# Kernel optimization log

Measured on AMD Instinct MI355X. Metric: run time of the kernel, lower is better.

## Reference

```python
import jax, jax.numpy as jnp
import numpy as np

B = 2; D = 256; NH = 8; NL = 4; HD = D // NH
K = 2; P = K * K; NV = 4; DFF = 1024
SHAPES = ((128, 128), (64, 64), (32, 32), (16, 16))
LV = sum(h * w for h, w in SHAPES)
START = np.cumsum([0] + [h * w for h, w in SHAPES])[:-1].tolist()
EPS = 1e-5

# fixed 2x2 sampling kernel, matching _create_kernel_indices (even kernel branch)
_ind = np.linspace(-0.5, 0.5, K)
_ii, _jj = np.meshgrid(_ind, _ind, indexing='ij')
KERNEL = jnp.asarray(np.stack([_jj, _ii], -1).reshape(-1, 2) / K, jnp.float32)  # (P,2)


def _layer_norm(x, w, b):
    m = x.mean(-1, keepdims=True)
    v = ((x - m) ** 2).mean(-1, keepdims=True)
    return (x - m) * jax.lax.rsqrt(v + EPS) * w + b


def _box_attention(query, value, ref_windows, vpw, vpb, opw, opb, boxw, boxb, attw, attb):
    b, lq, _ = query.shape
    # value projection, split into heads: (b, NH, LV, HD)
    v = (value @ vpw.T + vpb).reshape(b, LV, NH, HD).transpose(0, 2, 1, 3)

    # attention weights: softmax over all (level, point) jointly per head
    aw = query @ attw.T + attb
    aw = jax.nn.softmax(aw.reshape(b, lq, NH, NL * P), -1).reshape(b, lq, NH, NL, P)

    # where to attend (with_rotation=False -> 4 offset variables, angle from ref)
    ob = (query @ boxw.T + boxb).reshape(b, lq, NH, NL, NV)
    rw = ref_windows[:, :, None, None, :]                    # (b,lq,1,1,7)
    ref_boxes = rw[..., jnp.array([0, 1, 3, 4])]
    angles = jnp.broadcast_to(rw[..., 6:7], (b, lq, NH, NL, 1))
    boxes = ref_boxes + ob / 8.0 * ref_boxes[..., jnp.array([2, 3, 2, 3])]
    center = boxes[..., None, :2]                            # (b,lq,NH,NL,1,2)
    size = boxes[..., None, 2:]
    c, s = jnp.cos(angles), jnp.sin(angles)
    rot = jnp.stack([c, -s, s, c], -1).reshape(b, lq, NH, NL, 1, 2, 2)
    g = KERNEL * jax.nn.relu(size)                           # (b,lq,NH,NL,P,2)
    grid = center + (g[..., None, :] * rot).sum(-1)          # (b,lq,NH,NL,P,2)

    # multi-level bilinear sampling (= grid_sample align_corners=False, zero pad)
    bidx = jnp.arange(b)[:, None, None, None]
    hidx = jnp.arange(NH)[None, None, :, None]
    out = jnp.zeros((b, lq, NH, HD), v.dtype)
    for lvl, (H, W) in enumerate(SHAPES):
        st = START[lvl]
        vl = v[:, :, st:st + H * W]                          # (b,NH,HW,HD)
        loc = grid[:, :, :, lvl]                             # (b,lq,NH,P,2)
        x = loc[..., 0] * W - 0.5
        y = loc[..., 1] * H - 0.5
        x0f = jnp.floor(x); y0f = jnp.floor(y)
        wx = x - x0f; wy = y - y0f
        x0 = x0f.astype(jnp.int32); y0 = y0f.astype(jnp.int32)
        acc = jnp.zeros((b, lq, NH, P, HD), v.dtype)
        corners = ((0, 0, (1 - wx) * (1 - wy)), (1, 0, wx * (1 - wy)),
                   (0, 1, (1 - wx) * wy), (1, 1, wx * wy))
        for dx, dy, wgt in corners:
            xi = x0 + dx; yi = y0 + dy
            valid = (xi >= 0) & (xi < W) & (yi >= 0) & (yi < H)
            idx = jnp.clip(yi, 0, H - 1) * W + jnp.clip(xi, 0, W - 1)
            samp = vl[bidx, hidx, idx]                       # (b,lq,NH,P,HD)
            acc = acc + (wgt * valid)[..., None] * samp
        out = out + jnp.einsum('blhp,blhpd->blhd', aw[:, :, :, lvl], acc)
    return out.reshape(b, lq, D) @ opw.T + opb


def setup_inputs() -> dict:
    key = jax.random.key(0)
    ks = jax.random.split(key, 20)
    def nrm(k, shape, fan_in):
        return jax.random.normal(k, shape, jnp.float32) * (1.0 / np.sqrt(fan_in))
    rw = jax.random.uniform(ks[2], (B, LV, 7), jnp.float32)
    # keep window sizes (cols 3,4,5) modest, like real BEV reference windows
    rw = rw.at[..., 3:6].multiply(0.2)
    return {
        'src': jax.random.normal(ks[0], (B, LV, D), jnp.float32),
        'pos': jax.random.normal(ks[1], (B, LV, D), jnp.float32),
        'src_shape': jnp.asarray(SHAPES, jnp.int32),
        'src_start_idx': jnp.asarray(START, jnp.int32),
        'ref_windows': rw,
        'vpw': nrm(ks[3], (D, D), D), 'vpb': jnp.zeros((D,), jnp.float32),
        'opw': nrm(ks[4], (D, D), D), 'opb': jnp.zeros((D,), jnp.float32),
        'boxw': nrm(ks[5], (NL * NH * NV, D), D) * 0.1,
        'boxb': jax.random.normal(ks[6], (NL * NH * NV,), jnp.float32) * 0.1,
        'attw': nrm(ks[7], (NH * NL * P, D), D),
        'attb': jnp.zeros((NH * NL * P,), jnp.float32),
        'lin1_w': nrm(ks[8], (DFF, D), D), 'lin1_b': jnp.zeros((DFF,), jnp.float32),
        'lin2_w': nrm(ks[9], (D, DFF), DFF), 'lin2_b': jnp.zeros((D,), jnp.float32),
        'ln1_w': jnp.ones((D,), jnp.float32), 'ln1_b': jnp.zeros((D,), jnp.float32),
        'ln2_w': jnp.ones((D,), jnp.float32), 'ln2_b': jnp.zeros((D,), jnp.float32),
    }


def reference(src, pos, src_shape, src_start_idx, ref_windows,
              vpw, vpb, opw, opb, boxw, boxb, attw, attb,
              lin1_w, lin1_b, lin2_w, lin2_b, ln1_w, ln1_b, ln2_w, ln2_b):
    # level shapes/starts are static (SHAPES/START constants); src_shape /
    # src_start_idx are accepted for signature fidelity.
    src2 = _box_attention(src + pos, src, ref_windows,
                          vpw, vpb, opw, opb, boxw, boxb, attw, attb)
    src = _layer_norm(src + src2, ln1_w, ln1_b)
    ffn = jax.nn.relu(src @ lin1_w.T + lin1_b) @ lin2_w.T + lin2_b
    return _layer_norm(src + ffn, ln2_w, ln2_b)
```

## Files before the change

kernel.cpp:

```cpp
#include <hip/hip_runtime.h>
#include <stdint.h>

typedef unsigned short u16;
typedef __attribute__((ext_vector_type(8))) short short8;
typedef __attribute__((ext_vector_type(4))) float f32x4;

#define D_    256
#define NH_   8
#define HD_   32
#define LV_   21760
#define DFF_  1024
#define EPS_  1e-5f
#define MH_   21760
#define MT_   43520

__device__ __forceinline__ float bf2f(u16 u) {
    union { uint32_t i; float f; } x; x.i = ((uint32_t)u) << 16; return x.f;
}
__device__ __forceinline__ u16 f2bf(float f) {
    union { float f; uint32_t i; } x; x.f = f;
    uint32_t r = x.i + 0x7FFFu + ((x.i >> 16) & 1u);
    return (u16)(r >> 16);
}
__device__ __forceinline__ uint32_t pk2(float a, float b) {
    return (uint32_t)f2bf(a) | ((uint32_t)f2bf(b) << 16);
}
__device__ __forceinline__ float blo(uint32_t u) {
    union { uint32_t i; float f; } x; x.i = u << 16; return x.f;
}
__device__ __forceinline__ float bhi(uint32_t u) {
    union { uint32_t i; float f; } x; x.i = u & 0xffff0000u; return x.f;
}
__device__ __forceinline__ void cv8(u16* dst, float4 a, float4 b) {
    uint4 r;
    r.x = pk2(a.x, a.y); r.y = pk2(a.z, a.w);
    r.z = pk2(b.x, b.y); r.w = pk2(b.z, b.w);
    *(uint4*)dst = r;
}
__device__ __forceinline__ void gload16(const u16* g, u16* l) {
    __builtin_amdgcn_global_load_lds(
        (const __attribute__((address_space(1))) uint32_t*)g,
        (__attribute__((address_space(3))) uint32_t*)l, 16, 0, 0);
}

__global__ __launch_bounds__(256) void k_cvt2(const float* __restrict__ in1, u16* __restrict__ out1,
                                              const float* __restrict__ in2, u16* __restrict__ out2) {
    int i = blockIdx.x * 256 + threadIdx.x;
    const float* in = (i < 65536) ? in1 : in2;
    u16* out = (i < 65536) ? out1 : out2;
    const int j = i & 65535;
    float4 v = ((const float4*)in)[j];
    uint2 r; r.x = pk2(v.x, v.y); r.y = pk2(v.z, v.w);
    *(uint2*)(out + (size_t)j * 4) = r;
}

__global__ __launch_bounds__(256) void k_proj(
        const float* __restrict__ src, const float* __restrict__ pos,
        const float* __restrict__ vpw, const float* __restrict__ vpb,
        const float* __restrict__ attw, const float* __restrict__ attb,
        const float* __restrict__ boxw, const float* __restrict__ boxb,
        u16* __restrict__ vout, u16* __restrict__ lgout) {
    __shared__ u16 As[2][64 * 32];
    __shared__ u16 Bs[2][64 * 32];
    const int t = threadIdx.x;
    const int l = t & 63, w = t >> 6;
    const int m0 = blockIdx.x * 64;
    const int by = blockIdx.y;
    const bool isv = by < 4;
    const int n0 = (by & 3) * 64;
    const float* Bsrc = isv ? (vpw + (size_t)n0 * 256)
                            : ((n0 < 128) ? (attw + (size_t)n0 * 256)
                                          : (boxw + (size_t)(n0 - 128) * 256));
    const float* bsrc = isv ? (vpb + n0)
                            : ((n0 < 128) ? (attb + n0) : (boxb + (n0 - 128)));
    const int sr = t >> 2, sc = t & 3;
    const int wslot = sr * 32 + ((sc ^ ((sr >> 1) & 3)) << 3);
    const float* gAs = src + (size_t)(m0 + sr) * 256 + sc * 8;
    const float* gAp = pos + (size_t)(m0 + sr) * 256 + sc * 8;
    const float* gB  = Bsrc + (size_t)sr * 256 + sc * 8;
    const int fr = l & 15, fg = l >> 4;
    const int wm = w >> 1, wn = w & 1;

    f32x4 acc[2][2];
    #pragma unroll
    for (int mi = 0; mi < 2; ++mi)
        #pragma unroll
        for (int ni = 0; ni < 2; ++ni)
            acc[mi][ni] = (f32x4){0.f, 0.f, 0.f, 0.f};

    {
        float4 a0 = *(const float4*)gAs, a1 = *(const float4*)(gAs + 4);
        if (!isv) {
            float4 p0 = *(const float4*)gAp, p1 = *(const float4*)(gAp + 4);
            a0.x += p0.x; a0.y += p0.y; a0.z += p0.z; a0.w += p0.w;
            a1.x += p1.x; a1.y += p1.y; a1.z += p1.z; a1.w += p1.w;
        }
        cv8(&As[0][wslot], a0, a1);
        cv8(&Bs[0][wslot], *(const float4*)gB, *(const float4*)(gB + 4));
    }
    __syncthreads();

    for (int kt = 0; kt < 8; ++kt) {
        const int cur = kt & 1;
        float4 na0, na1, nb0, nb1;
        if (kt < 7) {
            na0 = *(const float4*)(gAs + (kt + 1) * 32);
            na1 = *(const float4*)(gAs + (kt + 1) * 32 + 4);
            if (!isv) {
                float4 p0 = *(const float4*)(gAp + (kt + 1) * 32);
                float4 p1 = *(const float4*)(gAp + (kt + 1) * 32 + 4);
                na0.x += p0.x; na0.y += p0.y; na0.z += p0.z; na0.w += p0.w;
                na1.x += p1.x; na1.y += p1.y; na1.z += p1.z; na1.w += p1.w;
            }
            nb0 = *(const float4*)(gB + (kt + 1) * 32);
            nb1 = *(const float4*)(gB + (kt + 1) * 32 + 4);
        }
        short8 af[2], bfr[2];
        #pragma unroll
        for (int mi = 0; mi < 2; ++mi) {
            const int r = wm * 32 + mi * 16 + fr;
            af[mi] = *(const short8*)&As[cur][r * 32 + ((fg ^ ((r >> 1) & 3)) << 3)];
        }
        #pragma unroll
        for (int ni = 0; ni < 2; ++ni) {
            const int r = wn * 32 + ni * 16 + fr;
            bfr[ni] = *(const short8*)&Bs[cur][r * 32 + ((fg ^ ((r >> 1) & 3)) << 3)];
        }
        #pragma unroll
        for (int mi = 0; mi < 2; ++mi)
            #pragma unroll
            for (int ni = 0; ni < 2; ++ni)
                acc[mi][ni] = __builtin_amdgcn_mfma_f32_16x16x32_bf16(af[mi], bfr[ni], acc[mi][ni], 0, 0, 0);
        if (kt < 7) {
            cv8(&As[cur ^ 1][wslot], na0, na1);
            cv8(&Bs[cur ^ 1][wslot], nb0, nb1);
            __syncthreads();
        }
    }
    if (isv) {
        const int b = m0 / LV_;
        #pragma unroll
        for (int ni = 0; ni < 2; ++ni) {
            const int n = n0 + wn * 32 + ni * 16 + fr;
            const float bv = bsrc[wn * 32 + ni * 16 + fr];
            const int h = n >> 5, hd = n & 31;
            #pragma unroll
            for (int mi = 0; mi < 2; ++mi) {
                #pragma unroll
                for (int q = 0; q < 4; ++q) {
                    const int m = m0 + wm * 32 + mi * 16 + fg * 4 + q;
                    const int lrow = m - b * LV_;
                    vout[((size_t)(b * NH_ + h) * LV_ + lrow) * HD_ + hd] = f2bf(acc[mi][ni][q] + bv);
                }
            }
        }
    } else {
        #pragma unroll
        for (int ni = 0; ni < 2; ++ni) {
            const int nl_ = wn * 32 + ni * 16 + fr;
            const int n = n0 + nl_;
            const float bv = bsrc[nl_];
            const int off = (n < 128) ? ((n >> 4) * 32 + (n & 15))
                                      : (((n - 128) >> 4) * 32 + 16 + ((n - 128) & 15));
            #pragma unroll
            for (int mi = 0; mi < 2; ++mi) {
                #pragma unroll
                for (int q = 0; q < 4; ++q) {
                    const int m = m0 + wm * 32 + mi * 16 + fg * 4 + q;
                    lgout[(size_t)m * 256 + off] = f2bf(acc[mi][ni][q] + bv);
                }
            }
        }
    }
}

__global__ __launch_bounds__(128, 8) void k_sample(
        const u16* __restrict__ lg, const float* __restrict__ refw,
        const u16* __restrict__ vws, u16* __restrict__ smp) {
    __shared__ float LG[8][2][36];
    __shared__ float RW[8][8];
    __shared__ __align__(16) uint2 CWI[16 * 68];
    const int t = threadIdx.x;
    const int bid = blockIdx.x;
    const int combo = bid & 7;
    const int idx = bid >> 3;
    const int b = combo >> 2, hp = combo & 3;
    const int h0 = hp * 2;
    const long gr0 = (long)b * LV_ + (long)idx * 8;
    const uint32_t PLANEB = (uint32_t)LV_ * HD_ * 2;

    {
        const int row = t >> 4, part = t & 15;
        const uint2 v = *(const uint2*)(lg + (size_t)(gr0 + row) * 256 + h0 * 32 + part * 4);
        const int hs = part >> 3, kk = (part & 7) * 4;
        LG[row][hs][kk]     = blo(v.x);
        LG[row][hs][kk + 1] = bhi(v.x);
        LG[row][hs][kk + 2] = blo(v.y);
        LG[row][hs][kk + 3] = bhi(v.y);
        if (t < 56) {
            int r2 = t / 7, k = t % 7;
            RW[r2][k] = refw[(gr0 + r2) * 7 + k];
        }
    }
    __syncthreads();
    if (t < 16) {
        const int row = t >> 1, hs = t & 1;
        float* a = LG[row][hs];
        float m = a[0];
        #pragma unroll
        for (int k = 1; k < 16; ++k) m = fmaxf(m, a[k]);
        float s = 0.f;
        float e[16];
        #pragma unroll
        for (int k = 0; k < 16; ++k) { e[k] = __expf(a[k] - m); s += e[k]; }
        const float inv = 1.f / s;
        #pragma unroll
        for (int k = 0; k < 16; ++k) a[k] = e[k] * inv;
    }
    __syncthreads();
    #pragma unroll
    for (int uu = 0; uu < 2; ++uu) {
        const int u = t + uu * 128;
        const int row = u >> 5, rem = u & 31;
        const int hs = rem >> 4, nl = (rem >> 2) & 3, p = rem & 3;
        const float rw0 = RW[row][0], rw1 = RW[row][1], rw3 = RW[row][3], rw4 = RW[row][4], ang = RW[row][6];
        const float ob0 = LG[row][hs][16 + nl * 4 + 0];
        const float ob1 = LG[row][hs][16 + nl * 4 + 1];
        const float ob2 = LG[row][hs][16 + nl * 4 + 2];
        const float ob3 = LG[row][hs][16 + nl * 4 + 3];
        const float cx = rw0 + ob0 * 0.125f * rw3;
        const float cy = rw1 + ob1 * 0.125f * rw4;
        const float bw = fmaxf(rw3 + ob2 * 0.125f * rw3, 0.f);
        const float bh = fmaxf(rw4 + ob3 * 0.125f * rw4, 0.f);
        const float kx = (p & 1) ? 0.25f : -0.25f;
        const float ky = (p >> 1) ? 0.25f : -0.25f;
        float sth, cth;
        __sincosf(ang, &sth, &cth);
        const float g0 = kx * bw, g1 = ky * bh;
        const float gx = cx + g0 * cth - g1 * sth;
        const float gy = cy + g0 * sth + g1 * cth;
        const int Wl = 128 >> nl;
        const int st = (65536 - (65536 >> (2 * nl))) / 3;
        const float x = gx * Wl - 0.5f, y = gy * Wl - 0.5f;
        const float xf = floorf(x), yf = floorf(y);
        const float wx = x - xf, wy = y - yf;
        const int x0 = (int)xf, y0 = (int)yf;
        const float awv = LG[row][hs][nl * 4 + p];
        const uint32_t hoff = hs ? PLANEB : 0u;
        uint2 cw[4];
        #pragma unroll
        for (int c4 = 0; c4 < 4; ++c4) {
            const int dx = c4 & 1, dy = c4 >> 1;
            const int xi = x0 + dx, yi = y0 + dy;
            const float wgt = (dx ? wx : 1.f - wx) * (dy ? wy : 1.f - wy);
            const bool valid = (xi >= 0) && (xi < Wl) && (yi >= 0) && (yi < Wl);
            const int xc = xi < 0 ? 0 : (xi > Wl - 1 ? Wl - 1 : xi);
            const int yc = yi < 0 ? 0 : (yi > Wl - 1 ? Wl - 1 : yi);
            const float wv = valid ? wgt * awv : 0.f;
            cw[c4].x = __float_as_uint(wv);
            cw[c4].y = (uint32_t)(st + yc * Wl + xc) * 64u + hoff;
        }
        const int g = row * 2 + hs, un = nl * 4 + p;
        uint2* d0 = &CWI[g * 68 + un * 2];
        *(uint4*)(d0)      = *(const uint4*)&cw[0];
        *(uint4*)(d0 + 34) = *(const uint4*)&cw[2];
    }
    __syncthreads();
    {
        const int e = t & 7, g = t >> 3;
        const int row = g >> 1, hs = g & 1;
        const char* vbp = (const char*)vws +
            (((size_t)(b * NH_ + h0) * LV_) * HD_ + e * 4) * 2;
        const uint2* cbase = &CWI[g * 68];
        float a0 = 0.f, a1 = 0.f, a2 = 0.f, a3 = 0.f;
        #pragma unroll 1
        for (int k = 0; k < 16; k += 2) {
            const uint4 c0 = *(const uint4*)&cbase[k * 2];
            const uint4 c1 = *(const uint4*)&cbase[34 + k * 2];
            const uint4 c2 = *(const uint4*)&cbase[(k + 1) * 2];
            const uint4 c3 = *(const uint4*)&cbase[34 + (k + 1) * 2];
            const uint2 d0 = *(const uint2*)(vbp + c0.y);
            const uint2 d1 = *(const uint2*)(vbp + c0.w);
            const uint2 d2 = *(const uint2*)(vbp + c1.y);
            const uint2 d3 = *(const uint2*)(vbp + c1.w);
            const uint2 d4 = *(const uint2*)(vbp + c2.y);
            const uint2 d5 = *(const uint2*)(vbp + c2.w);
            const uint2 d6 = *(const uint2*)(vbp + c3.y);
            const uint2 d7 = *(const uint2*)(vbp + c3.w);
            #define ACC8(WB, DD) do { \
                const float w_ = __uint_as_float(WB); \
                a0 += w_ * blo((DD).x); a1 += w_ * bhi((DD).x); \
                a2 += w_ * blo((DD).y); a3 += w_ * bhi((DD).y); \
            } while (0)
            ACC8(c0.x, d0); ACC8(c0.z, d1); ACC8(c1.x, d2); ACC8(c1.z, d3);
            ACC8(c2.x, d4); ACC8(c2.z, d5); ACC8(c3.x, d6); ACC8(c3.z, d7);
            #undef ACC8
        }
        uint2 o; o.x = pk2(a0, a1); o.y = pk2(a2, a3);
        *(uint2*)(smp + (size_t)(gr0 + row) * 256 + (h0 + hs) * 32 + e * 4) = o;
    }
}

__global__ __launch_bounds__(256) void k_oproj(
        const u16* __restrict__ A,
        const float* __restrict__ opw,
        const float* __restrict__ opb,
        const float* __restrict__ src,
        const float* __restrict__ lnw, const float* __restrict__ lnb,
        u16* __restrict__ out) {
    __shared__ char smem[36864];
    u16* As = (u16*)smem;
    u16* Bs = (u16*)(smem + 4096);
    float* Y = (float*)smem;
    const int t = threadIdx.x;
    const int l = t & 63, w = t >> 6;
    const int m0 = blockIdx.x * 32;
    const int sAr = t >> 2, sc = t & 3;
    const int aslot = sAr * 32 + ((sc ^ ((sAr >> 1) & 3)) << 3);
    const u16* gA = A + (size_t)(m0 + sAr) * 256 + sc * 8;
    const float* gB[4];
    int bslot[4];
    #pragma unroll
    for (int i = 0; i < 4; ++i) {
        const int r = (t >> 2) + i * 64;
        gB[i] = opw + (size_t)r * 256 + sc * 8;
        bslot[i] = r * 32 + ((sc ^ ((r >> 1) & 3)) << 3);
    }
    const int fr = l & 15, fg = l >> 4;

    f32x4 acc[2][4];
    #pragma unroll
    for (int mi = 0; mi < 2; ++mi)
        #pragma unroll
        for (int ni = 0; ni < 4; ++ni)
            acc[mi][ni] = (f32x4){0.f, 0.f, 0.f, 0.f};

    if (t < 128) *(uint4*)&As[aslot] = *(const uint4*)gA;
    #pragma unroll
    for (int i = 0; i < 4; ++i)
        cv8(&Bs[bslot[i]], *(const float4*)gB[i], *(const float4*)(gB[i] + 4));
    __syncthreads();

    for (int kt = 0; kt < 8; ++kt) {
        const int cur = kt & 1;
        uint4 na; float4 nb[4][2];
        if (kt < 7) {
            if (t < 128) na = *(const uint4*)(gA + (kt + 1) * 32);
            #pragma unroll
            for (int i = 0; i < 4; ++i) {
                nb[i][0] = *(const float4*)(gB[i] + (kt + 1) * 32);
                nb[i][1] = *(const float4*)(gB[i] + (kt + 1) * 32 + 4);
            }
        }
        short8 af[2], bfr[4];
        #pragma unroll
        for (int mi = 0; mi < 2; ++mi) {
            const int r = mi * 16 + fr;
            af[mi] = *(const short8*)&As[cur * 1024 + r * 32 + ((fg ^ ((r >> 1) & 3)) << 3)];
        }
        #pragma unroll
        for (int ni = 0; ni < 4; ++ni) {
            const int r = w * 64 + ni * 16 + fr;
            bfr[ni] = *(const short8*)&Bs[cur * 8192 + r * 32 + ((fg ^ ((r >> 1) & 3)) << 3)];
        }
        #pragma unroll
        for (int mi = 0; mi < 2; ++mi)
            #pragma unroll
            for (int ni = 0; ni < 4; ++ni)
                acc[mi][ni] = __builtin_amdgcn_mfma_f32_16x16x32_bf16(af[mi], bfr[ni], acc[mi][ni], 0, 0, 0);
        if (kt < 7) {
            if (t < 128) *(uint4*)&As[(cur ^ 1) * 1024 + aslot] = na;
            #pragma unroll
            for (int i = 0; i < 4; ++i)
                cv8(&Bs[(cur ^ 1) * 8192 + bslot[i]], nb[i][0], nb[i][1]);
            __syncthreads();
        }
    }
    __syncthreads();
    #pragma unroll
    for (int ni = 0; ni < 4; ++ni) {
        const int n = w * 64 + ni * 16 + fr;
        const float bv = opb[n];
        #pragma unroll
        for (int mi = 0; mi < 2; ++mi) {
            #pragma unroll
            for (int q = 0; q < 4; ++q) {
                const int ml = mi * 16 + fg * 4 + q;
                Y[ml * 256 + n] = acc[mi][ni][q] + bv + src[(size_t)(m0 + ml) * 256 + n];
            }
        }
    }
    __syncthreads();
    for (int rr = 0; rr < 8; ++rr) {
        const int m = w * 8 + rr;
        const float v0 = Y[m * 256 + l];
        const float v1 = Y[m * 256 + 64 + l];
        const float v2 = Y[m * 256 + 128 + l];
        const float v3 = Y[m * 256 + 192 + l];
        float s1 = v0 + v1 + v2 + v3;
        float s2 = v0 * v0 + v1 * v1 + v2 * v2 + v3 * v3;
        #pragma unroll
        for (int off = 32; off; off >>= 1) {
            s1 += __shfl_xor(s1, off);
            s2 += __shfl_xor(s2, off);
        }
        const float mean = s1 * (1.f / 256.f);
        const float var = s2 * (1.f / 256.f) - mean * mean;
        const float rs = rsqrtf(var + EPS_);
        const size_t ob = (size_t)(m0 + m) * 256;
        out[ob + l]       = f2bf((v0 - mean) * rs * lnw[l]       + lnb[l]);
        out[ob + 64 + l]  = f2bf((v1 - mean) * rs * lnw[64 + l]  + lnb[64 + l]);
        out[ob + 128 + l] = f2bf((v2 - mean) * rs * lnw[128 + l] + lnb[128 + l]);
        out[ob + 192 + l] = f2bf((v3 - mean) * rs * lnw[192 + l] + lnb[192 + l]);
    }
}

__global__ __launch_bounds__(256) void k_gemm1(
        const u16* __restrict__ A, const u16* __restrict__ Bw,
        const float* __restrict__ bias, u16* __restrict__ H) {
    __shared__ u16 As[2][128 * 32];
    __shared__ u16 Bs[2][128 * 32];
    const int t = threadIdx.x;
    const int l = t & 63, w = t >> 6;
    const int m0 = blockIdx.x * 128, n0 = blockIdx.y * 128;
    const int r0 = t >> 2, c0 = t & 3;
    const int gc = c0 ^ ((r0 >> 1) & 3);
    const u16* gA0 = A  + (size_t)(m0 + r0) * 256 + gc * 8;
    const u16* gA1 = A  + (size_t)(m0 + r0 + 64) * 256 + gc * 8;
    const u16* gB0 = Bw + (size_t)(n0 + r0) * 256 + gc * 8;
    const u16* gB1 = Bw + (size_t)(n0 + r0 + 64) * 256 + gc * 8;
    const int lbase = w * 512;
    const int fr = l & 15, fg = l >> 4;
    const int wm = w >> 1, wn = w & 1;

    f32x4 acc[4][4];
    #pragma unroll
    for (int mi = 0; mi < 4; ++mi)
        #pragma unroll
        for (int ni = 0; ni < 4; ++ni)
            acc[mi][ni] = (f32x4){0.f, 0.f, 0.f, 0.f};

    #define STAGE1(buf, kt) do { \
        gload16(gA0 + (kt) * 32, &As[buf][lbase]); \
        gload16(gA1 + (kt) * 32, &As[buf][2048 + lbase]); \
        gload16(gB0 + (kt) * 32, &Bs[buf][lbase]); \
        gload16(gB1 + (kt) * 32, &Bs[buf][2048 + lbase]); \
    } while (0)

    STAGE1(0, 0);
    __syncthreads();

    for (int kt = 0; kt < 8; ++kt) {
        const int cur = kt & 1;
        if (kt < 7) STAGE1(cur ^ 1, kt + 1);
        short8 af[4], bfr[4];
        #pragma unroll
        for (int mi = 0; mi < 4; ++mi) {
            const int r = wm * 64 + mi * 16 + fr;
            af[mi] = *(const short8*)&As[cur][r * 32 + ((fg ^ ((r >> 1) & 3)) << 3)];
        }
        #pragma unroll
        for (int ni = 0; ni < 4; ++ni) {
            const int r = wn * 64 + ni * 16 + fr;
            bfr[ni] = *(const short8*)&Bs[cur][r * 32 + ((fg ^ ((r >> 1) & 3)) << 3)];
        }
        #pragma unroll
        for (int mi = 0; mi < 4; ++mi)
            #pragma unroll
            for (int ni = 0; ni < 4; ++ni)
                acc[mi][ni] = __builtin_amdgcn_mfma_f32_16x16x32_bf16(af[mi], bfr[ni], acc[mi][ni], 0, 0, 0);
        __syncthreads();
    }
    #undef STAGE1
    #pragma unroll
    for (int ni = 0; ni < 4; ++ni) {
        const int n = n0 + wn * 64 + ni * 16 + fr;
        const float bv = bias[n];
        #pragma unroll
        for (int mi = 0; mi < 4; ++mi) {
            #pragma unroll
            for (int q = 0; q < 4; ++q) {
                const int m = m0 + wm * 64 + mi * 16 + fg * 4 + q;
                const float v = acc[mi][ni][q] + bv;
                H[(size_t)m * 1024 + n] = f2bf(fmaxf(v, 0.f));
            }
        }
    }
}

__global__ __launch_bounds__(256) void k_gemm2(
        const u16* __restrict__ A, const u16* __restrict__ Bw,
        const float* __restrict__ bias, const u16* __restrict__ resid,
        const float* __restrict__ lnw, const float* __restrict__ lnb,
        float* __restrict__ out) {
    __shared__ char smem[36864];
    u16* As = (u16*)smem;
    u16* Bs = (u16*)(smem + 4096);
    float* Y = (float*)smem;
    const int t = threadIdx.x;
    const int l = t & 63, w = t >> 6;
    const int m0 = blockIdx.x * 32;
    const int r0 = t >> 2, c0 = t & 3;
    const int gc = c0 ^ ((r0 >> 1) & 3);
    const u16* gA = A + (size_t)(m0 + r0) * 1024 + gc * 8;
    const u16* gBp[4];
    #pragma unroll
    for (int i = 0; i < 4; ++i)
        gBp[i] = Bw + (size_t)(i * 64 + r0) * 1024 + gc * 8;
    const int lbase = w * 512;
    const int fr = l & 15, fg = l >> 4;

    f32x4 acc[2][4];
    #pragma unroll
    for (int mi = 0; mi < 2; ++mi)
        #pragma unroll
        for (int ni = 0; ni < 4; ++ni)
            acc[mi][ni] = (f32x4){0.f, 0.f, 0.f, 0.f};

    #define STAGE2(buf, kt) do { \
        if (t < 128) gload16(gA + (kt) * 32, &As[(buf) * 1024 + lbase]); \
        gload16(gBp[0] + (kt) * 32, &Bs[(buf) * 8192 + lbase]); \
        gload16(gBp[1] + (kt) * 32, &Bs[(buf) * 8192 + 2048 + lbase]); \
        gload16(gBp[2] + (kt) * 32, &Bs[(buf) * 8192 + 4096 + lbase]); \
        gload16(gBp[3] + (kt) * 32, &Bs[(buf) * 8192 + 6144 + lbase]); \
    } while (0)

    STAGE2(0, 0);
    __syncthreads();

    for (int kt = 0; kt < 32; ++kt) {
        const int cur = kt & 1;
        if (kt < 31) STAGE2(cur ^ 1, kt + 1);
        short8 af[2], bfr[4];
        #pragma unroll
        for (int mi = 0; mi < 2; ++mi) {
            const int r = mi * 16 + fr;
            af[mi] = *(const short8*)&As[cur * 1024 + r * 32 + ((fg ^ ((r >> 1) & 3)) << 3)];
        }
        #pragma unroll
        for (int ni = 0; ni < 4; ++ni) {
            const int r = w * 64 + ni * 16 + fr;
            bfr[ni] = *(const short8*)&Bs[cur * 8192 + r * 32 + ((fg ^ ((r >> 1) & 3)) << 3)];
        }
        #pragma unroll
        for (int mi = 0; mi < 2; ++mi)
            #pragma unroll
            for (int ni = 0; ni < 4; ++ni)
                acc[mi][ni] = __builtin_amdgcn_mfma_f32_16x16x32_bf16(af[mi], bfr[ni], acc[mi][ni], 0, 0, 0);
        __syncthreads();
    }
    #undef STAGE2
    #pragma unroll
    for (int ni = 0; ni < 4; ++ni) {
        const int n = w * 64 + ni * 16 + fr;
        const float bv = bias[n];
        #pragma unroll
        for (int mi = 0; mi < 2; ++mi) {
            #pragma unroll
            for (int q = 0; q < 4; ++q) {
                const int ml = mi * 16 + fg * 4 + q;
                Y[ml * 256 + n] = acc[mi][ni][q] + bv + bf2f(resid[(size_t)(m0 + ml) * 256 + n]);
            }
        }
    }
    __syncthreads();
    for (int rr = 0; rr < 8; ++rr) {
        const int m = w * 8 + rr;
        const float v0 = Y[m * 256 + l];
        const float v1 = Y[m * 256 + 64 + l];
        const float v2 = Y[m * 256 + 128 + l];
        const float v3 = Y[m * 256 + 192 + l];
        float s1 = v0 + v1 + v2 + v3;
        float s2 = v0 * v0 + v1 * v1 + v2 * v2 + v3 * v3;
        #pragma unroll
        for (int off = 32; off; off >>= 1) {
            s1 += __shfl_xor(s1, off);
            s2 += __shfl_xor(s2, off);
        }
        const float mean = s1 * (1.f / 256.f);
        const float var = s2 * (1.f / 256.f) - mean * mean;
        const float rs = rsqrtf(var + EPS_);
        const size_t ob = (size_t)(m0 + m) * 256;
        out[ob + l]        = (v0 - mean) * rs * lnw[l]        + lnb[l];
        out[ob + 64 + l]   = (v1 - mean) * rs * lnw[64 + l]   + lnb[64 + l];
        out[ob + 128 + l]  = (v2 - mean) * rs * lnw[128 + l]  + lnb[128 + l];
        out[ob + 192 + l]  = (v3 - mean) * rs * lnw[192 + l]  + lnb[192 + l];
    }
}

extern "C" void kernel_launch(void* const* d_in, const int* in_sizes, int n_in,
                              void* d_out, int out_size, void* d_ws, size_t ws_size,
                              hipStream_t stream) {
    const float* src  = (const float*)d_in[0];
    const float* pos  = (const float*)d_in[1];
    const float* refw = (const float*)d_in[4];
    const float* vpw  = (const float*)d_in[5];
    const float* vpb  = (const float*)d_in[6];
    const float* opw  = (const float*)d_in[7];
    const float* opb  = (const float*)d_in[8];
    const float* boxw = (const float*)d_in[9];
    const float* boxb = (const float*)d_in[10];
    const float* attw = (const float*)d_in[11];
    const float* attb = (const float*)d_in[12];
    const float* l1w  = (const float*)d_in[13];
    const float* l1b  = (const float*)d_in[14];
    const float* l2w  = (const float*)d_in[15];
    const float* l2b  = (const float*)d_in[16];
    const float* ln1w = (const float*)d_in[17];
    const float* ln1b = (const float*)d_in[18];
    const float* ln2w = (const float*)d_in[19];
    const float* ln2b = (const float*)d_in[20];

    u16*   vws    = (u16*)d_ws;
    u16*   l1wb   = (u16*)d_ws;
    u16*   l2wb   = (u16*)((char*)d_ws + 524288);
    u16*   logitsb= (u16*)((char*)d_ws + 22282240u);
    u16*   src1b  = (u16*)((char*)d_ws + 22282240u);
    u16*   Hbf    = (u16*)((char*)d_ws + 44564480u);
    u16*   smp    = (u16*)((char*)d_ws + 66846720u);

    hipLaunchKernelGGL(k_proj, dim3(680, 8), dim3(256), 0, stream,
                       src, pos, vpw, vpb, attw, attb, boxw, boxb, vws, logitsb);
    hipLaunchKernelGGL(k_sample, dim3(21760), dim3(128), 0, stream, logitsb, refw, vws, smp);
    hipLaunchKernelGGL(k_cvt2, dim3(512), dim3(256), 0, stream, l1w, l1wb, l2w, l2wb);
    hipLaunchKernelGGL(k_oproj, dim3(1360), dim3(256), 0, stream,
                       smp, opw, opb, src, ln1w, ln1b, src1b);
    for (int h = 0; h < 2; ++h) {
        const u16* Ah = src1b + (size_t)h * MH_ * 256;
        float* outh   = (float*)d_out + (size_t)h * MH_ * 256;
        hipLaunchKernelGGL(k_gemm1, dim3(170, 8), dim3(256), 0, stream, Ah, l1wb, l1b, Hbf);
        hipLaunchKernelGGL(k_gemm2, dim3(680), dim3(256), 0, stream, Hbf, l2wb, l2b, Ah, ln2w, ln2b, outh);
    }
}
```

Before: 322.0 us.

## Split projection into value and logits kernels with A-tile resident in LDS

Replaces the combined projection kernel, which tiled over N blocks and reloaded and reconverted the src/pos rows once per N tile, with two kernels. Each new kernel loads a 32-row, full-K A tile into LDS once and loops over all four 64-column weight slices. The goal is to cut the redundant global reads and fp32-to-bf16 conversion of the activations. The cost is smaller M tiles, fewer MFMAs per B load, and an extra kernel launch, while weight tiles are still streamed per block.

```diff
diff --git a/kernel.cpp b/kernel.cpp
--- a/kernel.cpp
+++ b/kernel.cpp
@@ -54,121 +54,147 @@
     *(uint2*)(out + (size_t)j * 4) = r;
 }
 
-__global__ __launch_bounds__(256) void k_proj(
-        const float* __restrict__ src, const float* __restrict__ pos,
-        const float* __restrict__ vpw, const float* __restrict__ vpb,
-        const float* __restrict__ attw, const float* __restrict__ attb,
-        const float* __restrict__ boxw, const float* __restrict__ boxb,
-        u16* __restrict__ vout, u16* __restrict__ lgout) {
-    __shared__ u16 As[2][64 * 32];
+__global__ __launch_bounds__(256) void k_vproj(
+        const float* __restrict__ src, const float* __restrict__ vpw,
+        const float* __restrict__ vpb, u16* __restrict__ vout) {
+    __shared__ u16 Asl[32 * 256];
     __shared__ u16 Bs[2][64 * 32];
     const int t = threadIdx.x;
     const int l = t & 63, w = t >> 6;
-    const int m0 = blockIdx.x * 64;
-    const int by = blockIdx.y;
-    const bool isv = by < 4;
-    const int n0 = (by & 3) * 64;
-    const float* Bsrc = isv ? (vpw + (size_t)n0 * 256)
-                            : ((n0 < 128) ? (attw + (size_t)n0 * 256)
-                                          : (boxw + (size_t)(n0 - 128) * 256));
-    const float* bsrc = isv ? (vpb + n0)
-                            : ((n0 < 128) ? (attb + n0) : (boxb + (n0 - 128)));
+    const int m0 = blockIdx.x * 32;
+    const int wm = w >> 1, wn = w & 1;
+    const int fr = l & 15, fg = l >> 4;
     const int sr = t >> 2, sc = t & 3;
     const int wslot = sr * 32 + ((sc ^ ((sr >> 1) & 3)) << 3);
-    const float* gAs = src + (size_t)(m0 + sr) * 256 + sc * 8;
-    const float* gAp = pos + (size_t)(m0 + sr) * 256 + sc * 8;
-    const float* gB  = Bsrc + (size_t)sr * 256 + sc * 8;
+    const int b = m0 / LV_;
+
+    #pragma unroll
+    for (int i = 0; i < 4; ++i) {
+        const int ii = t + i * 256;
+        const int row = ii >> 5, c8 = ii & 31;
+        const float* p = src + (size_t)(m0 + row) * 256 + c8 * 8;
+        cv8(&Asl[row * 256 + ((c8 ^ (row & 15)) << 3)],
+            *(const float4*)p, *(const float4*)(p + 4));
+    }
+    __syncthreads();
+
+    for (int s = 0; s < 4; ++s) {
+        const float* Bsl = vpw + (size_t)(s * 64) * 256;
+        const float* gB = Bsl + (size_t)sr * 256 + sc * 8;
+        f32x4 acc[2];
+        acc[0] = (f32x4){0.f, 0.f, 0.f, 0.f};
+        acc[1] = (f32x4){0.f, 0.f, 0.f, 0.f};
+        cv8(&Bs[0][wslot], *(const float4*)gB, *(const float4*)(gB + 4));
+        __syncthreads();
+        for (int kt = 0; kt < 8; ++kt) {
+            const int cur = kt & 1;
+            float4 nb0, nb1;
+            if (kt < 7) {
+                nb0 = *(const float4*)(gB + (kt + 1) * 32);
+                nb1 = *(const float4*)(gB + (kt + 1) * 32 + 4);
+            }
+            const int arow = wm * 16 + fr;
+            const short8 af = *(const short8*)&Asl[arow * 256 + (((kt * 4 + fg) ^ (arow & 15)) << 3)];
+            short8 bfr[2];
+            #pragma unroll
+            for (int ni = 0; ni < 2; ++ni) {
+                const int r = wn * 32 + ni * 16 + fr;
+                bfr[ni] = *(const short8*)&Bs[cur][r * 32 + ((fg ^ ((r >> 1) & 3)) << 3)];
+            }
+            #pragma unroll
+            for (int ni = 0; ni < 2; ++ni)
+                acc[ni] = __builtin_amdgcn_mfma_f32_16x16x32_bf16(af, bfr[ni], acc[ni], 0, 0, 0);
+            if (kt < 7) {
+                cv8(&Bs[cur ^ 1][wslot], nb0, nb1);
+                __syncthreads();
+            }
+        }
+        #pragma unroll
+        for (int ni = 0; ni < 2; ++ni) {
+            const int n = s * 64 + wn * 32 + ni * 16 + fr;
+            const float bv = vpb[n];
+            const int h = n >> 5, hd = n & 31;
+            #pragma unroll
+            for (int q = 0; q < 4; ++q) {
+                const int m = m0 + wm * 16 + fg * 4 + q;
+                const int lrow = m - b * LV_;
+                vout[((size_t)(b * NH_ + h) * LV_ + lrow) * HD_ + hd] = f2bf(acc[ni][q] + bv);
+            }
+        }
+    }
+}
+
+__global__ __launch_bounds__(256) void k_logits(
+        const float* __restrict__ src, const float* __restrict__ pos,
+        const float* __restrict__ attw, const float* __restrict__ attb,
+        const float* __restrict__ boxw, const float* __restrict__ boxb,
+        u16* __restrict__ lgout) {
+    __shared__ u16 Asl[32 * 256];
+    __shared__ u16 Bs[2][64 * 32];
+    const int t = threadIdx.x;
+    const int l = t & 63, w = t >> 6;
+    const int m0 = blockIdx.x * 32;
+    const int wm = w >> 1, wn = w & 1;
     const int fr = l & 15, fg = l >> 4;
-    const int wm = w >> 1, wn = w & 1;
-
-    f32x4 acc[2][2];
-    #pragma unroll
-    for (int mi = 0; mi < 2; ++mi)
-        #pragma unroll
-        for (int ni = 0; ni < 2; ++ni)
-            acc[mi][ni] = (f32x4){0.f, 0.f, 0.f, 0.f};
-
-    {
-        float4 a0 = *(const float4*)gAs, a1 = *(const float4*)(gAs + 4);
-        if (!isv) {
-            float4 p0 = *(const float4*)gAp, p1 = *(const float4*)(gAp + 4);
-            a0.x += p0.x; a0.y += p0.y; a0.z += p0.z; a0.w += p0.w;
-            a1.x += p1.x; a1.y += p1.y; a1.z += p1.z; a1.w += p1.w;
-        }
-        cv8(&As[0][wslot], a0, a1);
+    const int sr = t >> 2, sc = t & 3;
+    const int wslot = sr * 32 + ((sc ^ ((sr >> 1) & 3)) << 3);
+
+    #pragma unroll
+    for (int i = 0; i < 4; ++i) {
+        const int ii = t + i * 256;
+        const int row = ii >> 5, c8 = ii & 31;
+        const float* p  = src + (size_t)(m0 + row) * 256 + c8 * 8;
+        const float* p2 = pos + (size_t)(m0 + row) * 256 + c8 * 8;
+        float4 a0 = *(const float4*)p,  a1 = *(const float4*)(p + 4);
+        float4 q0 = *(const float4*)p2, q1 = *(const float4*)(p2 + 4);
+        a0.x += q0.x; a0.y += q0.y; a0.z += q0.z; a0.w += q0.w;
+        a1.x += q1.x; a1.y += q1.y; a1.z += q1.z; a1.w += q1.w;
+        cv8(&Asl[row * 256 + ((c8 ^ (row & 15)) << 3)], a0, a1);
+    }
+    __syncthreads();
+
+    for (int s = 0; s < 4; ++s) {
+        const float* Bsl = (s < 2) ? (attw + (size_t)(s * 64) * 256)
+                                   : (boxw + (size_t)(s * 64 - 128) * 256);
+        const float* gB = Bsl + (size_t)sr * 256 + sc * 8;
+        f32x4 acc[2];
+        acc[0] = (f32x4){0.f, 0.f, 0.f, 0.f};
+        acc[1] = (f32x4){0.f, 0.f, 0.f, 0.f};
         cv8(&Bs[0][wslot], *(const float4*)gB, *(const float4*)(gB + 4));
-    }
-    __syncthreads();
-
-    for (int kt = 0; kt < 8; ++kt) {
-        const int cur = kt & 1;
-        float4 na0, na1, nb0, nb1;
-        if (kt < 7) {
-            na0 = *(const float4*)(gAs + (kt + 1) * 32);
-            na1 = *(const float4*)(gAs + (kt + 1) * 32 + 4);
-            if (!isv) {
-                float4 p0 = *(const float4*)(gAp + (kt + 1) * 32);
-                float4 p1 = *(const float4*)(gAp + (kt + 1) * 32 + 4);
-                na0.x += p0.x; na0.y += p0.y; na0.z += p0.z; na0.w += p0.w;
-                na1.x += p1.x; na1.y += p1.y; na1.z += p1.z; na1.w += p1.w;
-            }
-            nb0 = *(const float4*)(gB + (kt + 1) * 32);
-            nb1 = *(const float4*)(gB + (kt + 1) * 32 + 4);
-        }
-        short8 af[2], bfr[2];
-        #pragma unroll
-        for (int mi = 0; mi < 2; ++mi) {
-            const int r = wm * 32 + mi * 16 + fr;
-            af[mi] = *(const short8*)&As[cur][r * 32 + ((fg ^ ((r >> 1) & 3)) << 3)];
+        __syncthreads();
+        for (int kt = 0; kt < 8; ++kt) {
+            const int cur = kt & 1;
+            float4 nb0, nb1;
+            if (kt < 7) {
+                nb0 = *(const float4*)(gB + (kt + 1) * 32);
+                nb1 = *(const float4*)(gB + (kt + 1) * 32 + 4);
+            }
+            const int arow = wm * 16 + fr;
+            const short8 af = *(const short8*)&Asl[arow * 256 + (((kt * 4 + fg) ^ (arow & 15)) << 3)];
+            short8 bfr[2];
+            #pragma unroll
+            for (int ni = 0; ni < 2; ++ni) {
+                const int r = wn * 32 + ni * 16 + fr;
+                bfr[ni] = *(const short8*)&Bs[cur][r * 32 + ((fg ^ ((r >> 1) & 3)) << 3)];
+            }
+            #pragma unroll
+            for (int ni = 0; ni < 2; ++ni)
+                acc[ni] = __builtin_amdgcn_mfma_f32_16x16x32_bf16(af, bfr[ni], acc[ni], 0, 0, 0);
+            if (kt < 7) {
+                cv8(&Bs[cur ^ 1][wslot], nb0, nb1);
+                __syncthreads();
+            }
         }
         #pragma unroll
         for (int ni = 0; ni < 2; ++ni) {
-            const int r = wn * 32 + ni * 16 + fr;
-            bfr[ni] = *(const short8*)&Bs[cur][r * 32 + ((fg ^ ((r >> 1) & 3)) << 3)];
-        }
-        #pragma unroll
-        for (int mi = 0; mi < 2; ++mi)
-            #pragma unroll
-            for (int ni = 0; ni < 2; ++ni)
-                acc[mi][ni] = __builtin_amdgcn_mfma_f32_16x16x32_bf16(af[mi], bfr[ni], acc[mi][ni], 0, 0, 0);
-        if (kt < 7) {
-            cv8(&As[cur ^ 1][wslot], na0, na1);
-            cv8(&Bs[cur ^ 1][wslot], nb0, nb1);
-            __syncthreads();
-        }
-    }
-    if (isv) {
-        const int b = m0 / LV_;
-        #pragma unroll
-        for (int ni = 0; ni < 2; ++ni) {
-            const int n = n0 + wn * 32 + ni * 16 + fr;
-            const float bv = bsrc[wn * 32 + ni * 16 + fr];
-            const int h = n >> 5, hd = n & 31;
-            #pragma unroll
-            for (int mi = 0; mi < 2; ++mi) {
-                #pragma unroll
-                for (int q = 0; q < 4; ++q) {
-                    const int m = m0 + wm * 32 + mi * 16 + fg * 4 + q;
-                    const int lrow = m - b * LV_;
-                    vout[((size_t)(b * NH_ + h) * LV_ + lrow) * HD_ + hd] = f2bf(acc[mi][ni][q] + bv);
-                }
-            }
-        }
-    } else {
-        #pragma unroll
-        for (int ni = 0; ni < 2; ++ni) {
-            const int nl_ = wn * 32 + ni * 16 + fr;
-            const int n = n0 + nl_;
-            const float bv = bsrc[nl_];
+            const int n = s * 64 + wn * 32 + ni * 16 + fr;
+            const float bv = (n < 128) ? attb[n] : boxb[n - 128];
             const int off = (n < 128) ? ((n >> 4) * 32 + (n & 15))
                                       : (((n - 128) >> 4) * 32 + 16 + ((n - 128) & 15));
             #pragma unroll
-            for (int mi = 0; mi < 2; ++mi) {
-                #pragma unroll
-                for (int q = 0; q < 4; ++q) {
-                    const int m = m0 + wm * 32 + mi * 16 + fg * 4 + q;
-                    lgout[(size_t)m * 256 + off] = f2bf(acc[mi][ni][q] + bv);
-                }
+            for (int q = 0; q < 4; ++q) {
+                const int m = m0 + wm * 16 + fg * 4 + q;
+                lgout[(size_t)m * 256 + off] = f2bf(acc[ni][q] + bv);
             }
         }
     }
@@ -619,8 +645,9 @@
     u16*   Hbf    = (u16*)((char*)d_ws + 44564480u);
     u16*   smp    = (u16*)((char*)d_ws + 66846720u);
 
-    hipLaunchKernelGGL(k_proj, dim3(680, 8), dim3(256), 0, stream,
-                       src, pos, vpw, vpb, attw, attb, boxw, boxb, vws, logitsb);
+    hipLaunchKernelGGL(k_vproj,  dim3(1360), dim3(256), 0, stream, src, vpw, vpb, vws);
+    hipLaunchKernelGGL(k_logits, dim3(1360), dim3(256), 0, stream,
+                       src, pos, attw, attb, boxw, boxb, logitsb);
     hipLaunchKernelGGL(k_sample, dim3(21760), dim3(128), 0, stream, logitsb, refw, vws, smp);
     hipLaunchKernelGGL(k_cvt2, dim3(512), dim3(256), 0, stream, l1w, l1wb, l2w, l2wb);
     hipLaunchKernelGGL(k_oproj, dim3(1360), dim3(256), 0, stream,
```

Measured after the change: 321.8 us. Within noise of the previous version (-0.1%).
